# Optimization experiments

Measured on AMD Instinct MI355X. Metric: run time of the kernel, lower is better.

Reference implementation:

```python
import jax, jax.numpy as jnp
import numpy as np

B, S, D, H = 1, 2048, 4096, 32
HD = D // H
THETA = 10000.0
IN_SCALE = 0.1   # input_scale buffer
Q_SCALE = 0.1    # q_proj_scale buffer
K_SCALE = 0.1    # k_proj_scale buffer
V_SCALE = 0.1    # v_proj_scale buffer
OUT_SCALE = 0.1  # out_input_scale buffer


def _fake_q(x, scale, lo, hi):
    # round-to-int + clamp, kept in float (faithful to int8 fake-quant)
    return jnp.clip(jnp.round(x / scale), lo, hi)


def _w4a8_linear(x, qw, w_scale, in_scale):
    # int8 fake-quantized activation x int4-valued weight, dequant output
    qx = _fake_q(x, in_scale, -128, 127)
    return jnp.einsum('bsd,od->bso', qx, qw) * (in_scale * w_scale)


def _rope_tables(position_ids):
    inv_freq = 1.0 / (THETA ** (jnp.arange(0, HD, 2, dtype=jnp.float32) / HD))
    ang = position_ids.astype(jnp.float32)[..., None] * inv_freq  # [B,S,HD/2]
    emb = jnp.concatenate([ang, ang], axis=-1)                     # [B,S,HD]
    return jnp.cos(emb)[:, None], jnp.sin(emb)[:, None]            # [B,1,S,HD]


def _rotate_half(x):
    return jnp.concatenate([-x[..., HD // 2:], x[..., :HD // 2]], axis=-1)


def setup_inputs() -> dict:
    key = jax.random.key(0)
    ks = jax.random.split(key, 9)
    hidden_states = jax.random.normal(ks[0], (B, S, D), jnp.float32)
    def int4_w(k):
        return jnp.round(jax.random.uniform(k, (D, D), jnp.float32, -8.0, 7.0))
    def ch_scale(k):
        return jax.random.uniform(k, (D,), jnp.float32, 0.01, 0.03)
    wq, wk, wv, wo = int4_w(ks[1]), int4_w(ks[2]), int4_w(ks[3]), int4_w(ks[4])
    sq_w, sk_w, sv_w, so_w = ch_scale(ks[5]), ch_scale(ks[6]), ch_scale(ks[7]), ch_scale(ks[8])
    position_ids = jnp.arange(S, dtype=jnp.int32)[None, :]
    causal = jnp.tril(jnp.ones((S, S), dtype=bool))
    attention_mask = jnp.where(causal, 0.0, -1e9).astype(jnp.float32)[None, None]
    return dict(hidden_states=hidden_states, wq=wq, wk=wk, wv=wv, wo=wo,
                sq_w=sq_w, sk_w=sk_w, sv_w=sv_w, so_w=so_w,
                attention_mask=attention_mask, position_ids=position_ids)


def reference(hidden_states, wq, wk, wv, wo, sq_w, sk_w, sv_w, so_w,
              attention_mask, position_ids):
    # W4A8 dequant projections
    q = _w4a8_linear(hidden_states, wq, sq_w, IN_SCALE)
    k = _w4a8_linear(hidden_states, wk, sk_w, IN_SCALE)
    v = _w4a8_linear(hidden_states, wv, sv_w, IN_SCALE)
    q = q.reshape(B, S, H, HD).transpose(0, 2, 1, 3)  # [B,H,S,HD]
    k = k.reshape(B, S, H, HD).transpose(0, 2, 1, 3)
    v = v.reshape(B, S, H, HD).transpose(0, 2, 1, 3)
    # RoPE
    cos, sin = _rope_tables(position_ids)
    q = q * cos + _rotate_half(q) * sin
    k = k * cos + _rotate_half(k) * sin
    # int8 fake-quant of q/k/v, then dequant before matmuls
    q = _fake_q(q, Q_SCALE, -128, 127)
    k = _fake_q(k, K_SCALE, -128, 127)
    v = _fake_q(v, V_SCALE, -128, 127)
    scores = jnp.einsum('bhqd,bhkd->bhqk', q * Q_SCALE, k * K_SCALE) / np.sqrt(HD)
    scores = scores + attention_mask
    attn = jax.nn.softmax(scores.astype(jnp.float32), axis=-1)
    out = jnp.einsum('bhqk,bhkd->bhqd', attn, v * V_SCALE)
    out = out.transpose(0, 2, 1, 3).reshape(B, S, D)
    # o_proj input re-quantized to int8 with out_input_scale (clamp -127..127)
    out_q = _fake_q(out, OUT_SCALE, -127, 127)
    attn_output = jnp.einsum('bsd,od->bso', out_q, wo) * (OUT_SCALE * so_w)
    return attn_output
```

## Files before the change

kernel.cpp:

```cpp
#include <hip/hip_runtime.h>
#include <math.h>
#include <stdint.h>

#define S_LEN 2048
#define D_DIM 4096
#define NHEAD 32
#define HDIM  128

typedef int      v4i __attribute__((ext_vector_type(4)));
typedef float    v4f __attribute__((ext_vector_type(4)));
typedef _Float16 v8h __attribute__((ext_vector_type(8)));

__device__ __forceinline__ float quant128(float x) {
  return fminf(fmaxf(rintf(x / 0.1f), -128.f), 127.f);
}
__device__ __forceinline__ void gl_lds16(const void* g, void* l) {
  __builtin_amdgcn_global_load_lds(
      (const __attribute__((address_space(1))) void*)g,
      (__attribute__((address_space(3))) void*)l, 16, 0, 0);
}

__global__ __launch_bounds__(256) void quant_hidden_k(const float* __restrict__ in,
                                                      int8_t* __restrict__ out) {
  const int idx = blockIdx.x * 256 + threadIdx.x;
  const float4 v = ((const float4*)in)[idx];
  const int q0 = (int)quant128(v.x), q1 = (int)quant128(v.y);
  const int q2 = (int)quant128(v.z), q3 = (int)quant128(v.w);
  ((int*)out)[idx] = (q0 & 0xff) | ((q1 & 0xff) << 8) | ((q2 & 0xff) << 16) | ((q3 & 0xff) << 24);
}

__global__ __launch_bounds__(256) void wconv3_k(const float* __restrict__ a,
                                                const float* __restrict__ b,
                                                const float* __restrict__ c,
                                                int8_t* __restrict__ out) {
  const int which = blockIdx.x >> 14;
  const int sub = blockIdx.x & 16383;
  const float* src = (which == 0) ? a : (which == 1) ? b : c;
  const int idx = sub * 256 + threadIdx.x;
  const float4 v = ((const float4*)src)[idx];
  const int q0 = __float2int_rn(v.x), q1 = __float2int_rn(v.y);
  const int q2 = __float2int_rn(v.z), q3 = __float2int_rn(v.w);
  ((int*)out)[(size_t)which * 4194304 + idx] =
      (q0 & 0xff) | ((q1 & 0xff) << 8) | ((q2 & 0xff) << 16) | ((q3 & 0xff) << 24);
}

__global__ __launch_bounds__(256) void wconv_k(const float* __restrict__ in,
                                               int8_t* __restrict__ out) {
  const int idx = blockIdx.x * 256 + threadIdx.x;
  const float4 v = ((const float4*)in)[idx];
  const int q0 = __float2int_rn(v.x), q1 = __float2int_rn(v.y);
  const int q2 = __float2int_rn(v.z), q3 = __float2int_rn(v.w);
  ((int*)out)[idx] = (q0 & 0xff) | ((q1 & 0xff) << 8) | ((q2 & 0xff) << 16) | ((q3 & 0xff) << 24);
}

__global__ __launch_bounds__(256) void rope_tab_k(const int* __restrict__ pos,
                                                  float* __restrict__ ct,
                                                  float* __restrict__ st) {
  const int idx = blockIdx.x * 256 + threadIdx.x;
  const int s = idx >> 6, j = idx & 63;
  const float inv = exp2f((float)j * -0.20762050593046016f);
  const float a = (float)pos[s] * inv;
  float si, c;
  sincosf(a, &si, &c);
  ct[idx] = c;
  st[idx] = si;
}

template <int MODE>
__global__ __launch_bounds__(512, 1) void gemm8p(
    const int8_t* __restrict__ A8, const int8_t* __restrict__ W8,
    const float* __restrict__ s0, const float* __restrict__ s1,
    const float* __restrict__ s2, const float* __restrict__ ctab,
    const float* __restrict__ stab, void* __restrict__ out0,
    void* __restrict__ out1, void* __restrict__ out2) {
  __shared__ __align__(16) int8_t LS[3 * 16384 + 3 * 32768];
  int8_t* const Abase = LS;
  int8_t* const Bbase = LS + 49152;

  const int t = threadIdx.x;
  const int w = t >> 6, lane = t & 63, g = lane >> 4, l15 = lane & 15;
  const int wm = w >> 2, wn = w & 3;

  const int nwg = gridDim.x;
  const int bid = blockIdx.x;
  const int lb = (bid & 7) * (nwg >> 3) + (bid >> 3);
  const int within = lb & 15, g16 = lb >> 4;
  const int bm = ((g16 & 3) * 4 + (within >> 2)) * 128;
  const int bn = ((g16 >> 2) * 4 + (within & 3)) * 256;

  const int rowo = lane >> 3;
  const int schunk = ((lane & 7) ^ rowo) * 16;
  const int8_t* srcA[2];
  const int8_t* srcB[4];
#pragma unroll
  for (int i = 0; i < 2; ++i)
    srcA[i] = A8 + (size_t)(bm + w * 16 + i * 8 + rowo) * D_DIM + schunk;
#pragma unroll
  for (int i = 0; i < 4; ++i)
    srcB[i] = W8 + (size_t)(bn + w * 32 + i * 8 + rowo) * D_DIM + schunk;

#define STAGE(KT, BI)                                                       \
  {                                                                         \
    const int kof_ = (KT) * 128;                                            \
    int8_t* Ad_ = Abase + (BI) * 16384 + w * 2048;                          \
    int8_t* Bd_ = Bbase + (BI) * 32768 + w * 4096;                          \
    _Pragma("unroll") for (int i_ = 0; i_ < 2; ++i_)                        \
        gl_lds16(srcA[i_] + kof_, Ad_ + i_ * 1024);                         \
    _Pragma("unroll") for (int i_ = 0; i_ < 4; ++i_)                        \
        gl_lds16(srcB[i_] + kof_, Bd_ + i_ * 1024);                         \
  }

  const int nc0 = (wn & 1) * 32 + (wn >> 1) * 128;

  v4i acc[4][4];
#pragma unroll
  for (int mi = 0; mi < 4; ++mi)
#pragma unroll
    for (int ni = 0; ni < 4; ++ni) acc[mi][ni] = (v4i){0, 0, 0, 0};

  STAGE(0, 0)
  STAGE(1, 1)

  for (int t3 = 0; t3 < 33; t3 += 3) {
#pragma unroll
    for (int u = 0; u < 3; ++u) {
      const int kt = t3 + u;
      if (kt < 32) {
        if (kt + 1 < 32)
          asm volatile("s_waitcnt vmcnt(6)" ::: "memory");
        else
          asm volatile("s_waitcnt vmcnt(0)" ::: "memory");
        __builtin_amdgcn_s_barrier();
        __builtin_amdgcn_sched_barrier(0);
        if (kt + 2 < 32) STAGE(kt + 2, ((u + 2) % 3))
        const int8_t* Ab = Abase + u * 16384;
        const int8_t* Bb = Bbase + u * 32768;
#pragma unroll
        for (int kk = 0; kk < 2; ++kk) {
          const int coff = (((kk << 2) | g) ^ (l15 & 7)) * 16;
          v4i bf[4], af[4];
#pragma unroll
          for (int ni = 0; ni < 4; ++ni) {
            const int nrow = nc0 + (ni & 1) * 16 + (ni >> 1) * 64 + l15;
            bf[ni] = *(const v4i*)(Bb + nrow * 128 + coff);
          }
#pragma unroll
          for (int mi = 0; mi < 4; ++mi)
            af[mi] = *(const v4i*)(Ab + (wm * 64 + mi * 16 + l15) * 128 + coff);
          __builtin_amdgcn_s_setprio(1);
#pragma unroll
          for (int mi = 0; mi < 4; ++mi)
#pragma unroll
            for (int ni = 0; ni < 4; ++ni)
              acc[mi][ni] =
                  __builtin_amdgcn_mfma_i32_16x16x64_i8(af[mi], bf[ni], acc[mi][ni], 0, 0, 0);
          __builtin_amdgcn_s_setprio(0);
        }
      }
    }
  }
#undef STAGE

  const int srow0 = bm + wm * 64;
  if (MODE == 1) {
    float* dst = (float*)out0;
#pragma unroll
    for (int ni = 0; ni < 4; ++ni) {
      const int col = bn + nc0 + (ni & 1) * 16 + (ni >> 1) * 64 + l15;
      const float sc = 0.1f * s0[col];
#pragma unroll
      for (int mi = 0; mi < 4; ++mi)
#pragma unroll
        for (int r = 0; r < 4; ++r)
          dst[(size_t)(srow0 + mi * 16 + g * 4 + r) * D_DIM + col] =
              (float)acc[mi][ni][r] * sc;
    }
  } else {
    const int seg = bn >> 12;
    const int bcol = bn & 4095;
    if (seg == 2) {
      _Float16* dst = (_Float16*)out2;
#pragma unroll
      for (int ni = 0; ni < 4; ++ni) {
        const int col = bcol + nc0 + (ni & 1) * 16 + (ni >> 1) * 64 + l15;
        const float scv = 0.1f * s2[col];
#pragma unroll
        for (int mi = 0; mi < 4; ++mi)
#pragma unroll
          for (int r = 0; r < 4; ++r) {
            const int s = srow0 + mi * 16 + g * 4 + r;
            dst[(size_t)col * S_LEN + s] = (_Float16)quant128((float)acc[mi][ni][r] * scv);
          }
      }
    } else {
      const float* wsc = seg ? s1 : s0;
      int8_t* dst = seg ? (int8_t*)out1 : (int8_t*)out0;
      const int hb = bcol + (wn >> 1) * 128;
#pragma unroll
      for (int ni = 0; ni < 2; ++ni) {
        const int dlo = (wn & 1) * 32 + ni * 16 + l15;
        const int clo = hb + dlo;
        const float sc0 = 0.1f * wsc[clo];
        const float sc1 = 0.1f * wsc[clo + 64];
#pragma unroll
        for (int mi = 0; mi < 4; ++mi)
#pragma unroll
          for (int r = 0; r < 4; ++r) {
            const int s = srow0 + mi * 16 + g * 4 + r;
            const float c = ctab[s * 64 + dlo];
            const float si = stab[s * 64 + dlo];
            const float x1 = (float)acc[mi][ni][r] * sc0;
            const float x2 = (float)acc[mi][ni + 2][r] * sc1;
            dst[(size_t)s * D_DIM + clo] = (int8_t)quant128(x1 * c - x2 * si);
            dst[(size_t)s * D_DIM + clo + 64] = (int8_t)quant128(x2 * c + x1 * si);
          }
      }
    }
  }
}

__global__ __launch_bounds__(256, 2) void attn_v7(
    const int8_t* __restrict__ q8, const int8_t* __restrict__ k8,
    const _Float16* __restrict__ vT, int8_t* __restrict__ o8) {
  __shared__ __align__(16) int8_t Kls[3][8192];
  __shared__ __align__(16) int8_t Vls[3][16384];
  const int j = 31 - blockIdx.x;
  const int h = blockIdx.y;
  const int t = threadIdx.x;
  const int w = t >> 6, lane = t & 63, g = lane >> 4, l15 = lane & 15;
  const int T = j + 1;
  const int q0 = (4 * j + w) * 16;
  const int q_lane = q0 + l15;
  const float SSCALE = 8.838834764831845e-4f;
  const v8h vones = {(_Float16)1, (_Float16)1, (_Float16)1, (_Float16)1,
                     (_Float16)1, (_Float16)1, (_Float16)1, (_Float16)1};

  int k_src[2], v_src[4], kv_dst[4];
#pragma unroll
  for (int i = 0; i < 2; ++i) {
    const int lin = i * 256 + t;
    const int s = lin >> 3;
    const int cs = (lin & 7) ^ (s & 7);
    const int key = ((s >> 5) & 1) * 32 + ((s >> 3) & 1) * 16 +
                    ((s >> 2) & 1) * 8 + ((s >> 4) & 1) * 4 + (s & 3);
    k_src[i] = key * D_DIM + cs * 16;
  }
#pragma unroll
  for (int i = 0; i < 4; ++i) {
    const int lin = i * 256 + t;
    const int d = lin >> 3;
    const int cs = (lin & 7) ^ (d & 7);
    v_src[i] = d * S_LEN + cs * 8;
    kv_dst[i] = lin * 16;
  }
  const int8_t* kbg = k8 + (size_t)h * HDIM;
  const _Float16* vbg = vT + (size_t)h * HDIM * S_LEN;

  auto stage = [&](int kt, int b) {
    const int8_t* ks = kbg + (size_t)kt * (64 * D_DIM);
    const _Float16* vs = vbg + kt * 64;
#pragma unroll
    for (int i = 0; i < 2; ++i) gl_lds16(ks + k_src[i], &Kls[b][kv_dst[i]]);
#pragma unroll
    for (int i = 0; i < 4; ++i) gl_lds16(vs + v_src[i], &Vls[b][kv_dst[i]]);
  };

  const v4i qa0 = *(const v4i*)(q8 + (size_t)q_lane * D_DIM + h * HDIM + g * 16);
  const v4i qa1 = *(const v4i*)(q8 + (size_t)q_lane * D_DIM + h * HDIM + 64 + g * 16);

  v4f o[8];
#pragma unroll
  for (int n = 0; n < 8; ++n) o[n] = (v4f){0.f, 0.f, 0.f, 0.f};
  v4f lacc = (v4f){0.f, 0.f, 0.f, 0.f};
  float m_i = -INFINITY;

  stage(0, 0);
  if (T > 1) stage(1, 1);

  int bi = 0;
  for (int kt = 0; kt < T; ++kt) {
    if (kt + 1 < T)
      asm volatile("s_waitcnt vmcnt(6)" ::: "memory");
    else
      asm volatile("s_waitcnt vmcnt(0)" ::: "memory");
    __builtin_amdgcn_s_barrier();
    __builtin_amdgcn_sched_barrier(0);
    if (kt + 2 < T) stage(kt + 2, bi >= 1 ? bi - 1 : bi + 2);

    const int ksw = (l15 & 7);
    float sc[4][4];
#pragma unroll
    for (int nt = 0; nt < 4; ++nt) {
      const int8_t* kr = &Kls[bi][(nt * 16 + l15) * 128];
      const v4i kb0 = *(const v4i*)(kr + ((g ^ ksw) * 16));
      const v4i kb1 = *(const v4i*)(kr + (((4 + g) ^ ksw) * 16));
      v4i c = (v4i){0, 0, 0, 0};
      c = __builtin_amdgcn_mfma_i32_16x16x64_i8(kb0, qa0, c, 0, 0, 0);
      c = __builtin_amdgcn_mfma_i32_16x16x64_i8(kb1, qa1, c, 0, 0, 0);
#pragma unroll
      for (int r = 0; r < 4; ++r) {
        float s = (float)c[r] * SSCALE;
        if (kt == T - 1) {
          const int key = kt * 64 + ((nt >> 1) << 5) + ((g >> 1) << 4) +
                          ((g & 1) << 3) + ((nt & 1) << 2) + r;
          if (key > q_lane) s = -1.0e30f;
        }
        sc[nt][r] = s;
      }
    }
    float mx = fmaxf(fmaxf(fmaxf(sc[0][0], sc[0][1]), fmaxf(sc[0][2], sc[0][3])),
                     fmaxf(fmaxf(sc[1][0], sc[1][1]), fmaxf(sc[1][2], sc[1][3])));
    mx = fmaxf(mx, fmaxf(fmaxf(fmaxf(sc[2][0], sc[2][1]), fmaxf(sc[2][2], sc[2][3])),
                         fmaxf(fmaxf(sc[3][0], sc[3][1]), fmaxf(sc[3][2], sc[3][3]))));
    mx = fmaxf(mx, __shfl_xor(mx, 16));
    mx = fmaxf(mx, __shfl_xor(mx, 32));
    const float mnew = fmaxf(m_i, mx);
    const float alpha = __expf(m_i - mnew);
    m_i = mnew;

    float p[4][4];
#pragma unroll
    for (int nt = 0; nt < 4; ++nt)
#pragma unroll
      for (int r = 0; r < 4; ++r) p[nt][r] = __expf(sc[nt][r] - m_i);

    v8h ph0, ph1;
#pragma unroll
    for (int e = 0; e < 8; ++e) {
      ph0[e] = (_Float16)p[e >> 2][e & 3];
      ph1[e] = (_Float16)p[2 + (e >> 2)][e & 3];
    }
    float a_r[4];
#pragma unroll
    for (int r = 0; r < 4; ++r)
      a_r[r] = __shfl(alpha, (lane & 48) | (g * 4 + r));
#pragma unroll
    for (int n = 0; n < 8; ++n)
#pragma unroll
      for (int r = 0; r < 4; ++r) o[n][r] *= a_r[r];
#pragma unroll
    for (int r = 0; r < 4; ++r) lacc[r] *= a_r[r];

    __builtin_amdgcn_s_setprio(1);
    lacc = __builtin_amdgcn_mfma_f32_16x16x32_f16(ph0, vones, lacc, 0, 0, 0);
    lacc = __builtin_amdgcn_mfma_f32_16x16x32_f16(ph1, vones, lacc, 0, 0, 0);
#pragma unroll
    for (int nt = 0; nt < 8; ++nt) {
      const int8_t* vr = &Vls[bi][(nt * 16 + l15) * 128];
      const v8h v0 = *(const v8h*)(vr + ((g ^ ksw) * 16));
      const v8h v1 = *(const v8h*)(vr + (((4 + g) ^ ksw) * 16));
      o[nt] = __builtin_amdgcn_mfma_f32_16x16x32_f16(ph0, v0, o[nt], 0, 0, 0);
      o[nt] = __builtin_amdgcn_mfma_f32_16x16x32_f16(ph1, v1, o[nt], 0, 0, 0);
    }
    __builtin_amdgcn_s_setprio(0);

    bi = (bi == 2) ? 0 : bi + 1;
  }

#pragma unroll
  for (int r = 0; r < 4; ++r) {
    const float rL = 1.0f / lacc[r];
    const size_t row = (size_t)(q0 + g * 4 + r) * D_DIM + h * HDIM;
#pragma unroll
    for (int nt = 0; nt < 8; ++nt) {
      const int q = (int)fminf(fmaxf(rintf(o[nt][r] * rL), -127.f), 127.f);
      o8[row + nt * 16 + l15] = (int8_t)q;
    }
  }
}

extern "C" void kernel_launch(void* const* d_in, const int* in_sizes, int n_in,
                              void* d_out, int out_size, void* d_ws, size_t ws_size,
                              hipStream_t stream) {
  (void)in_sizes; (void)n_in; (void)out_size; (void)ws_size;
  const float* hidden = (const float*)d_in[0];
  const float* wq = (const float*)d_in[1];
  const float* wk = (const float*)d_in[2];
  const float* wv = (const float*)d_in[3];
  const float* wo = (const float*)d_in[4];
  const float* sq = (const float*)d_in[5];
  const float* sk = (const float*)d_in[6];
  const float* sv = (const float*)d_in[7];
  const float* so = (const float*)d_in[8];
  const int* pos = (const int*)d_in[10];
  float* out = (float*)d_out;

  char* ws = (char*)d_ws;
  int8_t* h8 = (int8_t*)ws;
  int8_t* q8 = (int8_t*)(ws + (8ull << 20));
  int8_t* k8 = (int8_t*)(ws + (16ull << 20));
  _Float16* vT = (_Float16*)(ws + (24ull << 20));
  int8_t* w8a = (int8_t*)(ws + (40ull << 20));
  int8_t* w8b = (int8_t*)(ws + (56ull << 20));
  int8_t* w8c = (int8_t*)(ws + (72ull << 20));
  float* ctab = (float*)(ws + (88ull << 20));
  float* stab = (float*)(ws + (88ull << 20) + (512ull << 10));
  int8_t* o8 = h8;

  hipLaunchKernelGGL(rope_tab_k, dim3(512), dim3(256), 0, stream, pos, ctab, stab);
  hipLaunchKernelGGL(quant_hidden_k, dim3(8192), dim3(256), 0, stream, hidden, h8);
  hipLaunchKernelGGL(wconv3_k, dim3(49152), dim3(256), 0, stream, wq, wk, wv, w8a);

  hipLaunchKernelGGL((gemm8p<0>), dim3(768), dim3(512), 0, stream, h8, w8a,
                     sq, sk, sv, ctab, stab, (void*)q8, (void*)k8, (void*)vT);
  hipLaunchKernelGGL(wconv_k, dim3(16384), dim3(256), 0, stream, wo, w8a);
  hipLaunchKernelGGL(attn_v7, dim3(32, 32), dim3(256), 0, stream, q8, k8, vT, o8);
  hipLaunchKernelGGL((gemm8p<1>), dim3(256), dim3(512), 0, stream, o8, w8a,
                     so, so, so, ctab, stab, (void*)out, (void*)out, (void*)out);
}
```

Before: 523.0 us.

## Prefetch LDS fragments across barrier to overlap reads with MFMA in int8 GEMM

```diff
diff --git a/kernel.cpp b/kernel.cpp
--- a/kernel.cpp
+++ b/kernel.cpp
@@ -67,13 +67,13 @@
 }
 
 template <int MODE>
-__global__ __launch_bounds__(512, 1) void gemm8p(
-    const int8_t* __restrict__ A8, const int8_t* __restrict__ W8,
-    const float* __restrict__ s0, const float* __restrict__ s1,
-    const float* __restrict__ s2, const float* __restrict__ ctab,
-    const float* __restrict__ stab, void* __restrict__ out0,
-    void* __restrict__ out1, void* __restrict__ out2) {
-  __shared__ __align__(16) int8_t LS[3 * 16384 + 3 * 32768];
+__device__ __forceinline__ void gemm_body(
+    int8_t* __restrict__ LS, const int8_t* __restrict__ A8,
+    const int8_t* __restrict__ W8, const float* __restrict__ s0,
+    const float* __restrict__ s1, const float* __restrict__ s2,
+    const float* __restrict__ ctab, const float* __restrict__ stab,
+    void* __restrict__ out0, void* __restrict__ out1, void* __restrict__ out2,
+    int nwg) {
   int8_t* const Abase = LS;
   int8_t* const Bbase = LS + 49152;
 
@@ -81,7 +81,6 @@
   const int w = t >> 6, lane = t & 63, g = lane >> 4, l15 = lane & 15;
   const int wm = w >> 2, wn = w & 3;
 
-  const int nwg = gridDim.x;
   const int bid = blockIdx.x;
   const int lb = (bid & 7) * (nwg >> 3) + (bid >> 3);
   const int within = lb & 15, g16 = lb >> 4;
@@ -112,6 +111,33 @@
 
   const int nc0 = (wn & 1) * 32 + (wn >> 1) * 128;
 
+  const int coff0 = (g ^ (l15 & 7)) * 16;
+  const int coff1 = ((4 | g) ^ (l15 & 7)) * 16;
+  const int aoff = (wm * 64 + l15) * 128;
+  int boff[4];
+#pragma unroll
+  for (int ni = 0; ni < 4; ++ni)
+    boff[ni] = (nc0 + (ni & 1) * 16 + (ni >> 1) * 64 + l15) * 128;
+
+  v4i fa[4], fb[4];
+  v4i ga[4], gb[4];
+
+#define RD(FA, FB, BI, COFF)                                                \
+  {                                                                         \
+    const int8_t* Ab_ = Abase + (BI) * 16384;                               \
+    const int8_t* Bb_ = Bbase + (BI) * 32768;                               \
+    _Pragma("unroll") for (int mi_ = 0; mi_ < 4; ++mi_)                     \
+        FA[mi_] = *(const v4i*)(Ab_ + aoff + mi_ * 2048 + (COFF));          \
+    _Pragma("unroll") for (int ni_ = 0; ni_ < 4; ++ni_)                     \
+        FB[ni_] = *(const v4i*)(Bb_ + boff[ni_] + (COFF));                  \
+  }
+
+#define MM(FA, FB)                                                          \
+  _Pragma("unroll") for (int mi_ = 0; mi_ < 4; ++mi_)                       \
+  _Pragma("unroll") for (int ni_ = 0; ni_ < 4; ++ni_)                       \
+      acc[mi_][ni_] = __builtin_amdgcn_mfma_i32_16x16x64_i8(                \
+          FA[mi_], FB[ni_], acc[mi_][ni_], 0, 0, 0);
+
   v4i acc[4][4];
 #pragma unroll
   for (int mi = 0; mi < 4; ++mi)
@@ -120,46 +146,35 @@
 
   STAGE(0, 0)
   STAGE(1, 1)
+  asm volatile("s_waitcnt vmcnt(6)" ::: "memory");
+  __builtin_amdgcn_s_barrier();
+  __builtin_amdgcn_sched_barrier(0);
+  RD(fa, fb, 0, coff0)
 
   for (int t3 = 0; t3 < 33; t3 += 3) {
 #pragma unroll
     for (int u = 0; u < 3; ++u) {
       const int kt = t3 + u;
       if (kt < 32) {
-        if (kt + 1 < 32)
+        if (kt + 2 < 32) STAGE(kt + 2, ((u + 2) % 3))
+        RD(ga, gb, u, coff1)
+        __builtin_amdgcn_s_setprio(1);
+        MM(fa, fb)
+        MM(ga, gb)
+        __builtin_amdgcn_s_setprio(0);
+        if (kt + 2 < 32)
           asm volatile("s_waitcnt vmcnt(6)" ::: "memory");
         else
           asm volatile("s_waitcnt vmcnt(0)" ::: "memory");
         __builtin_amdgcn_s_barrier();
         __builtin_amdgcn_sched_barrier(0);
-        if (kt + 2 < 32) STAGE(kt + 2, ((u + 2) % 3))
-        const int8_t* Ab = Abase + u * 16384;
-        const int8_t* Bb = Bbase + u * 32768;
-#pragma unroll
-        for (int kk = 0; kk < 2; ++kk) {
-          const int coff = (((kk << 2) | g) ^ (l15 & 7)) * 16;
-          v4i bf[4], af[4];
-#pragma unroll
-          for (int ni = 0; ni < 4; ++ni) {
-            const int nrow = nc0 + (ni & 1) * 16 + (ni >> 1) * 64 + l15;
-            bf[ni] = *(const v4i*)(Bb + nrow * 128 + coff);
-          }
-#pragma unroll
-          for (int mi = 0; mi < 4; ++mi)
-            af[mi] = *(const v4i*)(Ab + (wm * 64 + mi * 16 + l15) * 128 + coff);
-          __builtin_amdgcn_s_setprio(1);
-#pragma unroll
-          for (int mi = 0; mi < 4; ++mi)
-#pragma unroll
-            for (int ni = 0; ni < 4; ++ni)
-              acc[mi][ni] =
-                  __builtin_amdgcn_mfma_i32_16x16x64_i8(af[mi], bf[ni], acc[mi][ni], 0, 0, 0);
-          __builtin_amdgcn_s_setprio(0);
-        }
+        if (kt + 1 < 32) RD(fa, fb, ((u + 1) % 3), coff0)
       }
     }
   }
 #undef STAGE
+#undef RD
+#undef MM
 
   const int srow0 = bm + wm * 64;
   if (MODE == 1) {
@@ -217,6 +232,24 @@
       }
     }
   }
+}
+
+__global__ __launch_bounds__(512, 1) void gemm_qkv(
+    const int8_t* __restrict__ A8, const int8_t* __restrict__ W8,
+    const float* __restrict__ s0, const float* __restrict__ s1,
+    const float* __restrict__ s2, const float* __restrict__ ctab,
+    const float* __restrict__ stab, void* __restrict__ out0,
+    void* __restrict__ out1, void* __restrict__ out2) {
+  __shared__ __align__(16) int8_t LS[3 * 16384 + 3 * 32768];
+  gemm_body<0>(LS, A8, W8, s0, s1, s2, ctab, stab, out0, out1, out2, 768);
+}
+
+__global__ __launch_bounds__(512, 1) void gemm_out(
+    const int8_t* __restrict__ A8, const int8_t* __restrict__ W8,
+    const float* __restrict__ s0, const float* __restrict__ ctab,
+    const float* __restrict__ stab, void* __restrict__ out0) {
+  __shared__ __align__(16) int8_t LS[3 * 16384 + 3 * 32768];
+  gemm_body<1>(LS, A8, W8, s0, s0, s0, ctab, stab, out0, out0, out0, 256);
 }
 
 __global__ __launch_bounds__(256, 2) void attn_v7(
@@ -401,10 +434,10 @@
   hipLaunchKernelGGL(quant_hidden_k, dim3(8192), dim3(256), 0, stream, hidden, h8);
   hipLaunchKernelGGL(wconv3_k, dim3(49152), dim3(256), 0, stream, wq, wk, wv, w8a);
 
-  hipLaunchKernelGGL((gemm8p<0>), dim3(768), dim3(512), 0, stream, h8, w8a,
+  hipLaunchKernelGGL(gemm_qkv, dim3(768), dim3(512), 0, stream, h8, w8a,
                      sq, sk, sv, ctab, stab, (void*)q8, (void*)k8, (void*)vT);
   hipLaunchKernelGGL(wconv_k, dim3(16384), dim3(256), 0, stream, wo, w8a);
   hipLaunchKernelGGL(attn_v7, dim3(32, 32), dim3(256), 0, stream, q8, k8, vT, o8);
-  hipLaunchKernelGGL((gemm8p<1>), dim3(256), dim3(512), 0, stream, o8, w8a,
-                     so, so, so, ctab, stab, (void*)out, (void*)out, (void*)out);
-}
+  hipLaunchKernelGGL(gemm_out, dim3(256), dim3(512), 0, stream, o8, w8a,
+                     so, ctab, stab, (void*)out);
+}
```

After: 522.9 us. About the same (-0.0%).
